# Kernel optimization log

Measured on AMD Instinct MI355X. Metric: run time of the kernel, lower is better.

Reference implementation:

```python
import jax, jax.numpy as jnp
import numpy as np

NUM_NODES = 100000
NUM_EDGES = 6400000


def setup_inputs() -> dict:
    key = jax.random.key(0)
    k1, k2 = jax.random.split(key)
    e = jax.random.normal(k1, (NUM_EDGES,), dtype=jnp.float32)
    edge_index = jax.random.randint(k2, (2, NUM_EDGES), 0, NUM_NODES, dtype=jnp.int64)
    return {"e": e, "edge_index": edge_index, "num_nodes": NUM_NODES}


def reference(e, edge_index, num_nodes):
    # Segment softmax of edge scores e over incoming edges per target node.
    target = edge_index[1]
    # scatter-amax with include_self=True on a -1e9-filled buffer
    e_max = jnp.full((num_nodes,), -1e9, dtype=e.dtype).at[target].max(e)
    exp_e = jnp.exp(e - e_max[target])
    sum_exp = jnp.zeros((num_nodes,), dtype=exp_e.dtype).at[target].add(exp_e)
    alpha = exp_e / (sum_exp[target] + 1e-16)
    return alpha
```

## Files before the change

### kernel.cpp

```cpp
#include <hip/hip_runtime.h>


static constexpr int NN   = 100000;
static constexpr int P    = 5;
static constexpr int PART = 20000;
static constexpr int NXCD = 8;
static constexpr int BPP  = 96;
static constexpr int NB   = P * BPP;
static constexpr int BT   = 1024;

__global__ __launch_bounds__(BT, 8)
void scatter_k(const float4* __restrict__ e4, const int4* __restrict__ t4,
               float* __restrict__ priv, int n4) {
    __shared__ float lsum[PART];
    const int xcd = blockIdx.x & (NXCD - 1);
    const int s   = blockIdx.x >> 3;
    const int p   = s % P;
    const int cb  = xcd + NXCD * (s / P);
    const int lo  = p * PART;

    for (int i = threadIdx.x; i < PART; i += BT) lsum[i] = 0.0f;
    __syncthreads();

    const int chunk = (n4 + BPP - 1) / BPP;
    const int beg   = cb * chunk;
    const int end   = min(beg + chunk, n4);

    for (int i0 = beg; i0 < end; i0 += 4 * BT) {
        float4 ev[4];
        int4   tv[4];
        bool   ok[4];
        #pragma unroll
        for (int u = 0; u < 4; ++u) {
            int i = i0 + u * BT + (int)threadIdx.x;
            ok[u] = (i < end);
            if (ok[u]) { ev[u] = e4[i]; tv[u] = t4[i]; }
        }
        #pragma unroll
        for (int u = 0; u < 4; ++u) {
            if (!ok[u]) continue;
            unsigned jx = (unsigned)(tv[u].x - lo);
            unsigned jy = (unsigned)(tv[u].y - lo);
            unsigned jz = (unsigned)(tv[u].z - lo);
            unsigned jw = (unsigned)(tv[u].w - lo);
            if (jx < (unsigned)PART) atomicAdd(&lsum[jx], __expf(ev[u].x));
            if (jy < (unsigned)PART) atomicAdd(&lsum[jy], __expf(ev[u].y));
            if (jz < (unsigned)PART) atomicAdd(&lsum[jz], __expf(ev[u].z));
            if (jw < (unsigned)PART) atomicAdd(&lsum[jw], __expf(ev[u].w));
        }
    }
    __syncthreads();

    float* dst = priv + (size_t)(cb * P + p) * PART;
    for (int i = threadIdx.x; i < PART; i += BT) dst[i] = lsum[i];
}

__global__ void reduce_k(const float* __restrict__ priv, float* __restrict__ rsum) {
    int n = blockIdx.x * blockDim.x + threadIdx.x;
    if (n >= NN) return;
    int pp = n / PART;
    int j  = n - pp * PART;
    const float* src = priv + (size_t)pp * PART + j;
    float s0 = 0.0f, s1 = 0.0f;
    for (int k = 0; k < BPP; k += 2) {
        s0 += src[(size_t)(k    ) * P * PART];
        s1 += src[(size_t)(k + 1) * P * PART];
    }
    rsum[n] = 1.0f / ((s0 + s1) + 1e-16f);
}

__global__ void norm_k(const float4* __restrict__ e4, const int4* __restrict__ t4,
                       const float* __restrict__ rsum, float4* __restrict__ out4,
                       int n4) {
    int half = n4 >> 1;
    int i = blockIdx.x * blockDim.x + threadIdx.x;
    if (i >= half) return;
    int i2 = i + half;
    float4 ea = e4[i],  eb = e4[i2];
    int4   ta = t4[i],  tb = t4[i2];
    float4 ra, rb;
    ra.x = __expf(ea.x) * rsum[ta.x];
    ra.y = __expf(ea.y) * rsum[ta.y];
    ra.z = __expf(ea.z) * rsum[ta.z];
    ra.w = __expf(ea.w) * rsum[ta.w];
    rb.x = __expf(eb.x) * rsum[tb.x];
    rb.y = __expf(eb.y) * rsum[tb.y];
    rb.z = __expf(eb.z) * rsum[tb.z];
    rb.w = __expf(eb.w) * rsum[tb.w];
    out4[i]  = ra;
    out4[i2] = rb;
}

extern "C" void kernel_launch(void* const* d_in, const int* in_sizes, int n_in,
                              void* d_out, int out_size, void* d_ws, size_t ws_size,
                              hipStream_t stream) {
    const float* e   = (const float*)d_in[0];
    const int*   idx = (const int*)d_in[1];
    const int E  = in_sizes[0];
    const int n4 = E / 4;

    const float4* e4 = (const float4*)e;
    const int4*   t4 = (const int4*)(idx + E);

    float*  rsum = (float*)d_ws;
    float*  priv = (float*)d_ws + NN;
    float4* out4 = (float4*)d_out;

    scatter_k<<<NB, BT, 0, stream>>>(e4, t4, priv, n4);
    reduce_k <<<(NN + 255) / 256, 256, 0, stream>>>(priv, rsum);
    norm_k   <<<(n4 / 2 + 255) / 256, 256, 0, stream>>>(e4, t4, rsum, out4, n4);
}
```

Before: 183.3 us.

## Fuse reduce and normalize via cooperative grid sync; branchless LDS atomics

Merges the per-node reduction and the edge normalization into one cooperative kernel separated by a grid-wide sync, which removes one launch and its gap. The scatter kernel replaces its per-edge partition branch with unconditional LDS atomics, sending out-of-range edges to padded dummy slots. This avoids divergence but makes every lane issue an atomic for every edge. The result is more LDS atomic traffic, plus the added cost of the grid sync.

```diff
diff --git a/kernel.cpp b/kernel.cpp
--- a/kernel.cpp
+++ b/kernel.cpp
@@ -1,4 +1,7 @@
 #include <hip/hip_runtime.h>
+#include <hip/hip_cooperative_groups.h>
+
+namespace cg = cooperative_groups;
 
 
 static constexpr int NN   = 100000;
@@ -12,14 +15,15 @@
 __global__ __launch_bounds__(BT, 8)
 void scatter_k(const float4* __restrict__ e4, const int4* __restrict__ t4,
                float* __restrict__ priv, int n4) {
-    __shared__ float lsum[PART];
+    __shared__ float lsum[PART + 64];
     const int xcd = blockIdx.x & (NXCD - 1);
     const int s   = blockIdx.x >> 3;
     const int p   = s % P;
     const int cb  = xcd + NXCD * (s / P);
     const int lo  = p * PART;
+    const int dummy = PART + (int)(threadIdx.x & 63);
 
-    for (int i = threadIdx.x; i < PART; i += BT) lsum[i] = 0.0f;
+    for (int i = threadIdx.x; i < PART + 64; i += BT) lsum[i] = 0.0f;
     __syncthreads();
 
     const int chunk = (n4 + BPP - 1) / BPP;
@@ -43,10 +47,14 @@
             unsigned jy = (unsigned)(tv[u].y - lo);
             unsigned jz = (unsigned)(tv[u].z - lo);
             unsigned jw = (unsigned)(tv[u].w - lo);
-            if (jx < (unsigned)PART) atomicAdd(&lsum[jx], __expf(ev[u].x));
-            if (jy < (unsigned)PART) atomicAdd(&lsum[jy], __expf(ev[u].y));
-            if (jz < (unsigned)PART) atomicAdd(&lsum[jz], __expf(ev[u].z));
-            if (jw < (unsigned)PART) atomicAdd(&lsum[jw], __expf(ev[u].w));
+            jx = (jx < (unsigned)PART) ? jx : (unsigned)dummy;
+            jy = (jy < (unsigned)PART) ? jy : (unsigned)dummy;
+            jz = (jz < (unsigned)PART) ? jz : (unsigned)dummy;
+            jw = (jw < (unsigned)PART) ? jw : (unsigned)dummy;
+            atomicAdd(&lsum[jx], __expf(ev[u].x));
+            atomicAdd(&lsum[jy], __expf(ev[u].y));
+            atomicAdd(&lsum[jz], __expf(ev[u].z));
+            atomicAdd(&lsum[jw], __expf(ev[u].w));
         }
     }
     __syncthreads();
@@ -55,40 +63,40 @@
     for (int i = threadIdx.x; i < PART; i += BT) dst[i] = lsum[i];
 }
 
-__global__ void reduce_k(const float* __restrict__ priv, float* __restrict__ rsum) {
-    int n = blockIdx.x * blockDim.x + threadIdx.x;
-    if (n >= NN) return;
-    int pp = n / PART;
-    int j  = n - pp * PART;
-    const float* src = priv + (size_t)pp * PART + j;
-    float s0 = 0.0f, s1 = 0.0f;
-    for (int k = 0; k < BPP; k += 2) {
-        s0 += src[(size_t)(k    ) * P * PART];
-        s1 += src[(size_t)(k + 1) * P * PART];
+static constexpr int RNB = 256;
+
+__global__ __launch_bounds__(BT)
+void rn_k(const float* __restrict__ priv, float* __restrict__ rsum,
+          const float4* __restrict__ e4, const int4* __restrict__ t4,
+          float4* __restrict__ out4, int n4) {
+    {
+        int n = blockIdx.x * BT + (int)threadIdx.x;
+        if (n < NN) {
+            int pp = n / PART;
+            int j  = n - pp * PART;
+            const float* src = priv + (size_t)pp * PART + j;
+            float s0 = 0.0f, s1 = 0.0f;
+            for (int k = 0; k < BPP; k += 2) {
+                s0 += src[(size_t)(k    ) * P * PART];
+                s1 += src[(size_t)(k + 1) * P * PART];
+            }
+            rsum[n] = 1.0f / ((s0 + s1) + 1e-16f);
+        }
     }
-    rsum[n] = 1.0f / ((s0 + s1) + 1e-16f);
-}
+    __threadfence();
+    cg::this_grid().sync();
 
-__global__ void norm_k(const float4* __restrict__ e4, const int4* __restrict__ t4,
-                       const float* __restrict__ rsum, float4* __restrict__ out4,
-                       int n4) {
-    int half = n4 >> 1;
-    int i = blockIdx.x * blockDim.x + threadIdx.x;
-    if (i >= half) return;
-    int i2 = i + half;
-    float4 ea = e4[i],  eb = e4[i2];
-    int4   ta = t4[i],  tb = t4[i2];
-    float4 ra, rb;
-    ra.x = __expf(ea.x) * rsum[ta.x];
-    ra.y = __expf(ea.y) * rsum[ta.y];
-    ra.z = __expf(ea.z) * rsum[ta.z];
-    ra.w = __expf(ea.w) * rsum[ta.w];
-    rb.x = __expf(eb.x) * rsum[tb.x];
-    rb.y = __expf(eb.y) * rsum[tb.y];
-    rb.z = __expf(eb.z) * rsum[tb.z];
-    rb.w = __expf(eb.w) * rsum[tb.w];
-    out4[i]  = ra;
-    out4[i2] = rb;
+    const int stride = RNB * BT;
+    for (int i = blockIdx.x * BT + (int)threadIdx.x; i < n4; i += stride) {
+        float4 e = e4[i];
+        int4   t = t4[i];
+        float4 r;
+        r.x = __expf(e.x) * rsum[t.x];
+        r.y = __expf(e.y) * rsum[t.y];
+        r.z = __expf(e.z) * rsum[t.z];
+        r.w = __expf(e.w) * rsum[t.w];
+        out4[i] = r;
+    }
 }
 
 extern "C" void kernel_launch(void* const* d_in, const int* in_sizes, int n_in,
@@ -97,7 +105,7 @@
     const float* e   = (const float*)d_in[0];
     const int*   idx = (const int*)d_in[1];
     const int E  = in_sizes[0];
-    const int n4 = E / 4;
+    int n4 = E / 4;
 
     const float4* e4 = (const float4*)e;
     const int4*   t4 = (const int4*)(idx + E);
@@ -107,6 +115,9 @@
     float4* out4 = (float4*)d_out;
 
     scatter_k<<<NB, BT, 0, stream>>>(e4, t4, priv, n4);
-    reduce_k <<<(NN + 255) / 256, 256, 0, stream>>>(priv, rsum);
-    norm_k   <<<(n4 / 2 + 255) / 256, 256, 0, stream>>>(e4, t4, rsum, out4, n4);
+
+    void* args[] = { (void*)&priv, (void*)&rsum, (void*)&e4, (void*)&t4,
+                     (void*)&out4, (void*)&n4 };
+    hipLaunchCooperativeKernel((const void*)rn_k, dim3(RNB), dim3(BT),
+                               args, 0, stream);
 }
```

Measured after the change: 440.6 us. +140.4%, slower.
